# Performance work log

Hardware: AMD Instinct MI355X
Metric: run time of the kernel (lower is better)

The kernel has to match this reference:

```python
import jax, jax.numpy as jnp
import numpy as np


def _gather_nbrs(atoms, edges):
    # atoms [B,N,F], edges [B,N,D] (neighbor indices) -> [B,N,D,F]
    return jax.vmap(lambda a, e: a[e])(atoms, edges)


def _linear(x, W, b):
    return x @ W + b


def setup_inputs() -> dict:
    key = jax.random.key(0)
    ks = jax.random.split(key, 32)
    B, Nm, Dm, Fa, Fb = 64, 64, 6, 37, 6      # molecules
    Np, Dp, Fp = 512, 12, 480                  # proteins
    HM, HP, NC = 128, 128, 1

    def rn(k, shape):
        return jax.random.normal(k, shape, jnp.float32) * 0.05

    return {
        'm_atoms': jax.random.normal(ks[0], (B, Nm, Fa), jnp.float32),
        'm_bonds': jax.random.normal(ks[1], (B, Nm, Dm, Fb), jnp.float32),
        'm_edges': jax.random.randint(ks[2], (B, Nm, Dm), 0, Nm, jnp.int32),
        'p_atoms': jax.random.normal(ks[3], (B, Np, Fp), jnp.float32),
        'p_edges': jax.random.randint(ks[4], (B, Np, Dp), 0, Np, jnp.int32),
        # GraphConv mol 1: in 43 = 37 atom + 6 bond
        'W1': rn(ks[5], (43, 128)), 'b1': jnp.zeros((128,), jnp.float32),
        # GraphConv mol 2: in 134 = 128 + 6
        'W2': rn(ks[6], (134, 128)), 'b2': jnp.zeros((128,), jnp.float32),
        # GraphConv_p 1/2
        'Wp1': rn(ks[7], (480, 200)), 'bp1': jnp.zeros((200,), jnp.float32),
        'Wp2': rn(ks[8], (200, 100)), 'bp2': jnp.zeros((100,), jnp.float32),
        # GraphOutput (134 -> hid_dim_m), GraphOutput_p (100 -> hid_dim_p)
        'Wo': rn(ks[9], (134, HM)), 'bo': jnp.zeros((HM,), jnp.float32),
        'Wop': rn(ks[10], (100, HP)), 'bop': jnp.zeros((HP,), jnp.float32),
        # FC stack
        'Wf1': rn(ks[11], (HM + HP, 100)), 'bf1': jnp.zeros((100,), jnp.float32),
        'Wf2': rn(ks[12], (100, 100)), 'bf2': jnp.zeros((100,), jnp.float32),
        'Wout': rn(ks[13], (100, NC)), 'bout': jnp.zeros((NC,), jnp.float32),
    }


def reference(m_atoms, m_bonds, m_edges, p_atoms, p_edges,
              W1, b1, W2, b2, Wp1, bp1, Wp2, bp2,
              Wo, bo, Wop, bop, Wf1, bf1, Wf2, bf2, Wout, bout):
    def gconv_mol(atoms, W, b):
        # self + summed-neighbor atom features, concat summed bond features
        nbr_sum = _gather_nbrs(atoms, m_edges).sum(2)           # [B,N,F]
        summed = jnp.concatenate([atoms + nbr_sum, m_bonds.sum(2)], axis=-1)
        return _linear(summed, W, b)

    def gconv_pro(atoms, W, b):
        nbr_sum = _gather_nbrs(atoms, p_edges).sum(2)
        return _linear(atoms + nbr_sum, W, b)

    a = jax.nn.relu(gconv_mol(m_atoms, W1, b1))
    a = jax.nn.relu(gconv_mol(a, W2, b2))
    # GraphOutput: tanh(linear(cat[atoms, bond_sum])) summed over atoms
    fp_m = jnp.tanh(_linear(jnp.concatenate([a, m_bonds.sum(2)], -1), Wo, bo)).sum(1)

    p = jax.nn.relu(gconv_pro(p_atoms, Wp1, bp1))
    p = jax.nn.relu(gconv_pro(p, Wp2, bp2))
    fp_p = jnp.tanh(_linear(p, Wop, bop)).sum(1)

    fp = jnp.concatenate([fp_m, fp_p], axis=1)
    # NOTE: source applies FC1 then FC2 with no activation in between
    fp = _linear(_linear(fp, Wf1, bf1), Wf2, bf2)
    return jax.nn.sigmoid(_linear(fp, Wout, bout))
```

## Files before the change

kernel.cpp:

```cpp
#include <hip/hip_runtime.h>
#include <cmath>

#define B   64
#define NM  64
#define DM  6
#define FA  37
#define FB  6
#define NP  512
#define DP  12
#define FPD 480
#define HM  128
#define HP  128

typedef _Float16 half8 __attribute__((ext_vector_type(8)));
typedef float f32x4 __attribute__((ext_vector_type(4)));

static const size_t OFF_FPP = 0;
static const size_t OFF_Z1  = OFF_FPP + (size_t)B*128;
static const size_t OFF_Z2  = OFF_Z1  + (size_t)32768*224/2;
static const size_t OFF_W16 = OFF_Z2  + (size_t)32768*128/2;
#define W16_WT1   0
#define W16_WT2   107520
#define W16_WTOP  136192
#define W16_MW1T  152576
#define W16_MW2T  160768
#define W16_MWOT  181248
#define W16_BP1   201728
#define W16_BP2   201952
#define W16_TOT   202080

__device__ __forceinline__ half8 load_a_frag(const float* p) {
    float4 f0 = *(const float4*)(p);
    float4 f1 = *(const float4*)(p + 4);
    half8 h;
    h[0] = (_Float16)f0.x; h[1] = (_Float16)f0.y; h[2] = (_Float16)f0.z; h[3] = (_Float16)f0.w;
    h[4] = (_Float16)f1.x; h[5] = (_Float16)f1.y; h[6] = (_Float16)f1.z; h[7] = (_Float16)f1.w;
    return h;
}

__global__ void k_prep(const float* __restrict__ Wp1, const float* __restrict__ Wp2,
                       const float* __restrict__ Wop,
                       const float* __restrict__ W1,  const float* __restrict__ W2,
                       const float* __restrict__ Wo,
                       const float* __restrict__ bp1, const float* __restrict__ bp2,
                       _Float16* __restrict__ w16) {
    int idx = blockIdx.x * 256 + threadIdx.x;
    if (idx < W16_WT2) {
        int n = idx / 480, k = idx % 480;
        w16[idx] = (n < 200) ? (_Float16)Wp1[k * 200 + n] : (_Float16)0.f;
    } else if (idx < W16_WTOP) {
        int r = idx - W16_WT2;
        int n = r / 224, k = r % 224;
        w16[idx] = (n < 100 && k < 200) ? (_Float16)Wp2[k * 100 + n] : (_Float16)0.f;
    } else if (idx < W16_MW1T) {
        int r = idx - W16_WTOP;
        int n = r >> 7, k = r & 127;
        w16[idx] = (k < 100) ? (_Float16)Wop[k * 128 + n] : (_Float16)0.f;
    } else if (idx < W16_MW2T) {
        int r = idx - W16_MW1T;
        int n = r >> 6, k = r & 63;
        w16[idx] = (k < 43) ? (_Float16)W1[k * 128 + n] : (_Float16)0.f;
    } else if (idx < W16_MWOT) {
        int r = idx - W16_MW2T;
        int n = r / 160, k = r % 160;
        w16[idx] = (k < 134) ? (_Float16)W2[k * 128 + n] : (_Float16)0.f;
    } else if (idx < W16_BP1) {
        int r = idx - W16_MWOT;
        int n = r / 160, k = r % 160;
        w16[idx] = (k < 134) ? (_Float16)Wo[k * 128 + n] : (_Float16)0.f;
    } else if (idx < W16_BP2) {
        int k = idx - W16_BP1;
        w16[idx] = (k < 200) ? (_Float16)bp1[k] : (_Float16)0.f;
    } else if (idx < W16_TOT) {
        int k = idx - W16_BP2;
        w16[idx] = (k < 100) ? (_Float16)bp2[k] : (_Float16)0.f;
    }
}

__global__ __launch_bounds__(256) void k_zp1(
        const float* __restrict__ A, const _Float16* __restrict__ Wt,
        _Float16* __restrict__ Z) {
    int tid = threadIdx.x, lane = tid & 63, wid = tid >> 6;
    int rw = wid & 1, cw = wid >> 1;
    int rbase = blockIdx.x * 32 + rw * 16;
    int cbase = cw * 112;
    int lr = lane & 15, q = lane >> 4, lkb = q * 8;
    f32x4 acc[7] = {};
    const float* Ar = A + (size_t)(rbase + lr) * FPD + lkb;
    for (int k0 = 0; k0 < FPD; k0 += 32) {
        half8 a = load_a_frag(Ar + k0);
        #pragma unroll
        for (int nt = 0; nt < 7; ++nt) {
            half8 b = *(const half8*)&Wt[(size_t)(cbase + nt * 16 + lr) * FPD + k0 + lkb];
            acc[nt] = __builtin_amdgcn_mfma_f32_16x16x32_f16(a, b, acc[nt], 0, 0, 0);
        }
    }
    int rj = q * 4;
    #pragma unroll
    for (int nt = 0; nt < 7; ++nt) {
        int col = cbase + nt * 16 + lr;
        #pragma unroll
        for (int j = 0; j < 4; ++j)
            Z[(size_t)(rbase + rj + j) * 224 + col] = (_Float16)acc[nt][j];
    }
}

__global__ __launch_bounds__(256) void k_zp2f(
        const _Float16* __restrict__ Z1, const int* __restrict__ edges,
        const _Float16* __restrict__ bp1h, const _Float16* __restrict__ Wt,
        _Float16* __restrict__ Z2) {
    int bid = blockIdx.x;
    int t = (bid & 7) * 64 + (bid >> 3);
    int tid = threadIdx.x, lane = tid & 63, wid = tid >> 6;
    int lr = lane & 15, q = lane >> 4, lkb = q * 8;
    int rbase = t * 64 + wid * 16;
    int gr = rbase + lr;
    int mb = gr >> 9, lrow = gr & 511;
    const int* ep = edges + (size_t)gr * DP;
    const _Float16* zb = Z1 + ((size_t)mb << 9) * 224;
    const _Float16* src[13];
    src[0] = zb + (size_t)lrow * 224;
    #pragma unroll
    for (int d = 0; d < 12; ++d) src[d + 1] = zb + (size_t)ep[d] * 224;

    f32x4 acc[7] = {};
    for (int k0 = 0; k0 < 224; k0 += 32) {
        int ko = k0 + lkb;
        half8 s = *(const half8*)(src[0] + ko);
        #pragma unroll
        for (int d = 1; d < 13; ++d) s = s + *(const half8*)(src[d] + ko);
        s = s + *(const half8*)(bp1h + ko);
        #pragma unroll
        for (int j = 0; j < 8; ++j) if (s[j] < (_Float16)0.f) s[j] = (_Float16)0.f;
        #pragma unroll
        for (int nt = 0; nt < 7; ++nt) {
            half8 b = *(const half8*)&Wt[(size_t)(nt * 16 + lr) * 224 + ko];
            acc[nt] = __builtin_amdgcn_mfma_f32_16x16x32_f16(s, b, acc[nt], 0, 0, 0);
        }
    }
    int rj = q * 4;
    #pragma unroll
    for (int nt = 0; nt < 7; ++nt) {
        int col = nt * 16 + lr;
        #pragma unroll
        for (int j = 0; j < 4; ++j)
            Z2[(size_t)(rbase + rj + j) * 128 + col] = (_Float16)acc[nt][j];
    }
}

__global__ __launch_bounds__(256) void k_pof(
        const _Float16* __restrict__ Z2, const int* __restrict__ edges,
        const _Float16* __restrict__ bp2h, const _Float16* __restrict__ Wt,
        const float* __restrict__ bop, float* __restrict__ fpp) {
    int bid = blockIdx.x;
    int t = (bid & 7) * 64 + (bid >> 3);
    int tid = threadIdx.x, lane = tid & 63, wid = tid >> 6;
    int lr = lane & 15, q = lane >> 4, lkb = q * 8;
    int rbase = t * 64 + wid * 16;
    int gr = rbase + lr;
    int mb = gr >> 9, lrow = gr & 511;
    const int* ep = edges + (size_t)gr * DP;
    const _Float16* zb = Z2 + ((size_t)mb << 9) * 128;
    const _Float16* src[13];
    src[0] = zb + (size_t)lrow * 128;
    #pragma unroll
    for (int d = 0; d < 12; ++d) src[d + 1] = zb + (size_t)ep[d] * 128;

    f32x4 acc[8] = {};
    for (int k0 = 0; k0 < 128; k0 += 32) {
        int ko = k0 + lkb;
        half8 s = *(const half8*)(src[0] + ko);
        #pragma unroll
        for (int d = 1; d < 13; ++d) s = s + *(const half8*)(src[d] + ko);
        s = s + *(const half8*)(bp2h + ko);
        #pragma unroll
        for (int j = 0; j < 8; ++j) if (s[j] < (_Float16)0.f) s[j] = (_Float16)0.f;
        #pragma unroll
        for (int nt = 0; nt < 8; ++nt) {
            half8 b = *(const half8*)&Wt[(size_t)(nt * 16 + lr) * 128 + ko];
            acc[nt] = __builtin_amdgcn_mfma_f32_16x16x32_f16(s, b, acc[nt], 0, 0, 0);
        }
    }
    #pragma unroll
    for (int nt = 0; nt < 8; ++nt) {
        int col = nt * 16 + lr;
        float bb = bop[col];
        float s = 0.f;
        #pragma unroll
        for (int j = 0; j < 4; ++j) s += tanhf(acc[nt][j] + bb);
        s += __shfl_xor(s, 16);
        s += __shfl_xor(s, 32);
        if (lane < 16) atomicAdd(&fpp[mb * 128 + col], s);
    }
}

#define P_ATOM 40
#define P_S1   72
#define P_A    136
#define P_S23  168
__global__ __launch_bounds__(512) void k_mol(
        const float* __restrict__ m_atoms, const float* __restrict__ m_bonds,
        const int* __restrict__ m_edges,
        const _Float16* __restrict__ W1t, const _Float16* __restrict__ W2t,
        const _Float16* __restrict__ Wot,
        const float* __restrict__ b1, const float* __restrict__ b2,
        const float* __restrict__ bo,
        const float* __restrict__ fpp,
        const float* __restrict__ Wf1, const float* __restrict__ bf1,
        const float* __restrict__ Wf2, const float* __restrict__ bf2,
        const float* __restrict__ Wout, const float* __restrict__ bout,
        float* __restrict__ out) {
    int b = blockIdx.x, tid = threadIdx.x;
    __shared__ __align__(16) float smem[11464];
    float*     atoms_sh = smem;
    _Float16*  a1  = (_Float16*)smem;
    _Float16*  S1  = (_Float16*)(smem + 4352);
    _Float16*  S23 = (_Float16*)(smem + 4352);
    float*     bond  = smem + 9728;
    int*       edg   = (int*)(smem + 10112);
    float*     red   = smem + 10496;
    float*     fcb   = smem + 11008;

    const float* ga = m_atoms + (size_t)b * NM * FA;
    for (int i = tid; i < NM * FA; i += 512)
        atoms_sh[(i / FA) * P_ATOM + (i % FA)] = ga[i];
    if (tid < NM * DM) edg[tid] = m_edges[b * NM * DM + tid];
    if (tid < NM * FB) {
        int r = tid / FB, j = tid % FB;
        float s = 0.f;
        #pragma unroll
        for (int d = 0; d < DM; ++d) s += m_bonds[((size_t)(b * NM + r) * DM + d) * FB + j];
        bond[tid] = s;
    }
    __syncthreads();

    for (int i = tid; i < 64 * 64; i += 512) {
        int r = i >> 6, k = i & 63;
        float v = 0.f;
        if (k < FA) {
            v = atoms_sh[r * P_ATOM + k];
            #pragma unroll
            for (int d = 0; d < DM; ++d) v += atoms_sh[edg[r * DM + d] * P_ATOM + k];
        } else if (k < FA + FB) {
            v = bond[r * FB + (k - FA)];
        }
        S1[r * P_S1 + k] = (_Float16)v;
    }
    __syncthreads();

    int lane = tid & 63, wid = tid >> 6;
    int rw = wid & 3, cw = wid >> 2;
    int rbase = rw * 16, cbase = cw * 64;
    int lr = lane & 15, lkb = (lane >> 4) * 8, rj = (lane >> 4) * 4;

    {
        f32x4 acc[4] = {};
        for (int k0 = 0; k0 < 64; k0 += 32) {
            half8 a = *(const half8*)&S1[(rbase + lr) * P_S1 + k0 + lkb];
            #pragma unroll
            for (int nt = 0; nt < 4; ++nt) {
                half8 bf = *(const half8*)&W1t[(cbase + nt * 16 + lr) * 64 + k0 + lkb];
                acc[nt] = __builtin_amdgcn_mfma_f32_16x16x32_f16(a, bf, acc[nt], 0, 0, 0);
            }
        }
        #pragma unroll
        for (int nt = 0; nt < 4; ++nt) {
            int col = cbase + nt * 16 + lr;
            float bb = b1[col];
            #pragma unroll
            for (int j = 0; j < 4; ++j)
                a1[(rbase + rj + j) * P_A + col] = (_Float16)fmaxf(acc[nt][j] + bb, 0.f);
        }
    }
    __syncthreads();

    for (int i = tid; i < 64 * 160; i += 512) {
        int r = i / 160, k = i % 160;
        float v = 0.f;
        if (k < 128) {
            v = (float)a1[r * P_A + k];
            #pragma unroll
            for (int d = 0; d < DM; ++d) v += (float)a1[edg[r * DM + d] * P_A + k];
        } else if (k < 134) {
            v = bond[r * FB + (k - 128)];
        }
        S23[r * P_S23 + k] = (_Float16)v;
    }
    __syncthreads();

    f32x4 acc2[4] = {};
    for (int k0 = 0; k0 < 160; k0 += 32) {
        half8 a = *(const half8*)&S23[(rbase + lr) * P_S23 + k0 + lkb];
        #pragma unroll
        for (int nt = 0; nt < 4; ++nt) {
            half8 bf = *(const half8*)&W2t[(cbase + nt * 16 + lr) * 160 + k0 + lkb];
            acc2[nt] = __builtin_amdgcn_mfma_f32_16x16x32_f16(a, bf, acc2[nt], 0, 0, 0);
        }
    }
    __syncthreads();

    #pragma unroll
    for (int nt = 0; nt < 4; ++nt) {
        int col = cbase + nt * 16 + lr;
        float bb = b2[col];
        #pragma unroll
        for (int j = 0; j < 4; ++j)
            S23[(rbase + rj + j) * P_S23 + col] = (_Float16)fmaxf(acc2[nt][j] + bb, 0.f);
    }
    for (int i = tid; i < 64 * 32; i += 512) {
        int r = i >> 5, k = 128 + (i & 31);
        S23[r * P_S23 + k] = (k < 134) ? (_Float16)bond[r * FB + (k - 128)] : (_Float16)0.f;
    }
    __syncthreads();

    {
        f32x4 acc3[4] = {};
        for (int k0 = 0; k0 < 160; k0 += 32) {
            half8 a = *(const half8*)&S23[(rbase + lr) * P_S23 + k0 + lkb];
            #pragma unroll
            for (int nt = 0; nt < 4; ++nt) {
                half8 bf = *(const half8*)&Wot[(cbase + nt * 16 + lr) * 160 + k0 + lkb];
                acc3[nt] = __builtin_amdgcn_mfma_f32_16x16x32_f16(a, bf, acc3[nt], 0, 0, 0);
            }
        }
        #pragma unroll
        for (int nt = 0; nt < 4; ++nt) {
            int col = cbase + nt * 16 + lr;
            float bb = bo[col];
            float s = 0.f;
            #pragma unroll
            for (int j = 0; j < 4; ++j) s += tanhf(acc3[nt][j] + bb);
            s += __shfl_xor(s, 16);
            s += __shfl_xor(s, 32);
            if (lane < 16) red[rw * 128 + col] = s;
        }
    }
    __syncthreads();

    if (tid < 128)       fcb[tid] = red[tid] + red[128 + tid] + red[256 + tid] + red[384 + tid];
    else if (tid < 256)  fcb[tid] = fpp[b * 128 + (tid - 128)];
    __syncthreads();
    if (tid < 100) {
        float acc = bf1[tid];
        for (int k = 0; k < 256; ++k) acc = fmaf(fcb[k], Wf1[k * 100 + tid], acc);
        fcb[256 + tid] = acc;
    }
    __syncthreads();
    if (tid < 100) {
        float acc = bf2[tid];
        for (int k = 0; k < 100; ++k) acc = fmaf(fcb[256 + k], Wf2[k * 100 + tid], acc);
        fcb[356 + tid] = acc;
    }
    __syncthreads();
    if (tid < 64) {
        float v = fcb[356 + tid] * Wout[tid];
        if (tid + 64 < 100) v += fcb[356 + tid + 64] * Wout[tid + 64];
        #pragma unroll
        for (int off = 32; off > 0; off >>= 1) v += __shfl_down(v, off);
        if (tid == 0) out[b] = 1.f / (1.f + expf(-(v + bout[0])));
    }
}

extern "C" void kernel_launch(void* const* d_in, const int* in_sizes, int n_in,
                              void* d_out, int out_size, void* d_ws, size_t ws_size,
                              hipStream_t stream) {
    const float* m_atoms = (const float*)d_in[0];
    const float* m_bonds = (const float*)d_in[1];
    const int*   m_edges = (const int*)  d_in[2];
    const float* p_atoms = (const float*)d_in[3];
    const int*   p_edges = (const int*)  d_in[4];
    const float* W1   = (const float*)d_in[5];  const float* b1   = (const float*)d_in[6];
    const float* W2   = (const float*)d_in[7];  const float* b2   = (const float*)d_in[8];
    const float* Wp1  = (const float*)d_in[9];  const float* bp1  = (const float*)d_in[10];
    const float* Wp2  = (const float*)d_in[11]; const float* bp2  = (const float*)d_in[12];
    const float* Wo   = (const float*)d_in[13]; const float* bo   = (const float*)d_in[14];
    const float* Wop  = (const float*)d_in[15]; const float* bop  = (const float*)d_in[16];
    const float* Wf1  = (const float*)d_in[17]; const float* bf1  = (const float*)d_in[18];
    const float* Wf2  = (const float*)d_in[19]; const float* bf2  = (const float*)d_in[20];
    const float* Wout = (const float*)d_in[21]; const float* bout = (const float*)d_in[22];

    float* ws   = (float*)d_ws;
    float* fpp  = ws + OFF_FPP;
    _Float16* z1  = (_Float16*)(ws + OFF_Z1);
    _Float16* z2  = (_Float16*)(ws + OFF_Z2);
    _Float16* w16 = (_Float16*)(ws + OFF_W16);

    hipMemsetAsync(fpp, 0, (size_t)B * 128 * sizeof(float), stream);
    k_prep<<<dim3((W16_TOT + 255) / 256), 256, 0, stream>>>(
        Wp1, Wp2, Wop, W1, W2, Wo, bp1, bp2, w16);

    k_zp1 <<<dim3(B * NP / 32), 256, 0, stream>>>(p_atoms, w16 + W16_WT1, z1);
    k_zp2f<<<dim3(B * NP / 64), 256, 0, stream>>>(z1, p_edges, w16 + W16_BP1,
                                                  w16 + W16_WT2, z2);
    k_pof <<<dim3(B * NP / 64), 256, 0, stream>>>(z2, p_edges, w16 + W16_BP2,
                                                  w16 + W16_WTOP, bop, fpp);

    k_mol <<<dim3(B), 512, 0, stream>>>(m_atoms, m_bonds, m_edges,
                                        w16 + W16_MW1T, w16 + W16_MW2T, w16 + W16_MWOT,
                                        b1, b2, bo, fpp,
                                        Wf1, bf1, Wf2, bf2, Wout, bout, (float*)d_out);
}
```

Before: 260.7 us.

## Tile-swizzle protein weights, pad Z1 stride, split gather GEMMs across waves

```diff
diff --git a/kernel.cpp b/kernel.cpp
--- a/kernel.cpp
+++ b/kernel.cpp
@@ -17,7 +17,7 @@
 
 static const size_t OFF_FPP = 0;
 static const size_t OFF_Z1  = OFF_FPP + (size_t)B*128;
-static const size_t OFF_Z2  = OFF_Z1  + (size_t)32768*224/2;
+static const size_t OFF_Z2  = OFF_Z1  + (size_t)32768*256/2;
 static const size_t OFF_W16 = OFF_Z2  + (size_t)32768*128/2;
 #define W16_WT1   0
 #define W16_WT2   107520
@@ -29,9 +29,7 @@
 #define W16_BP2   201952
 #define W16_TOT   202080
 
-__device__ __forceinline__ half8 load_a_frag(const float* p) {
-    float4 f0 = *(const float4*)(p);
-    float4 f1 = *(const float4*)(p + 4);
+__device__ __forceinline__ half8 cvt8(float4 f0, float4 f1) {
     half8 h;
     h[0] = (_Float16)f0.x; h[1] = (_Float16)f0.y; h[2] = (_Float16)f0.z; h[3] = (_Float16)f0.w;
     h[4] = (_Float16)f1.x; h[5] = (_Float16)f1.y; h[6] = (_Float16)f1.z; h[7] = (_Float16)f1.w;
@@ -46,15 +44,21 @@
                        _Float16* __restrict__ w16) {
     int idx = blockIdx.x * 256 + threadIdx.x;
     if (idx < W16_WT2) {
-        int n = idx / 480, k = idx % 480;
+        int c = idx / 7168, r = idx % 7168;
+        int nt = r >> 9, lr = (r >> 5) & 15, kin = r & 31;
+        int n = nt * 16 + lr, k = c * 32 + kin;
         w16[idx] = (n < 200) ? (_Float16)Wp1[k * 200 + n] : (_Float16)0.f;
     } else if (idx < W16_WTOP) {
-        int r = idx - W16_WT2;
-        int n = r / 224, k = r % 224;
+        int r0 = idx - W16_WT2;
+        int c = r0 >> 12, r = r0 & 4095;
+        int nt = r >> 9, lr = (r >> 5) & 15, kin = r & 31;
+        int n = nt * 16 + lr, k = c * 32 + kin;
         w16[idx] = (n < 100 && k < 200) ? (_Float16)Wp2[k * 100 + n] : (_Float16)0.f;
     } else if (idx < W16_MW1T) {
-        int r = idx - W16_WTOP;
-        int n = r >> 7, k = r & 127;
+        int r0 = idx - W16_WTOP;
+        int c = r0 >> 12, r = r0 & 4095;
+        int nt = r >> 9, lr = (r >> 5) & 15, kin = r & 31;
+        int n = nt * 16 + lr, k = c * 32 + kin;
         w16[idx] = (k < 100) ? (_Float16)Wop[k * 128 + n] : (_Float16)0.f;
     } else if (idx < W16_MW2T) {
         int r = idx - W16_MW1T;
@@ -83,25 +87,32 @@
     int tid = threadIdx.x, lane = tid & 63, wid = tid >> 6;
     int rw = wid & 1, cw = wid >> 1;
     int rbase = blockIdx.x * 32 + rw * 16;
-    int cbase = cw * 112;
-    int lr = lane & 15, q = lane >> 4, lkb = q * 8;
+    int lr = lane & 15, q = lane >> 4;
     f32x4 acc[7] = {};
-    const float* Ar = A + (size_t)(rbase + lr) * FPD + lkb;
-    for (int k0 = 0; k0 < FPD; k0 += 32) {
-        half8 a = load_a_frag(Ar + k0);
+    const float* Ar = A + (size_t)(rbase + lr) * FPD + q * 8;
+    const _Float16* Wb = Wt + (size_t)(cw * 7) * 512 + lr * 32 + q * 8;
+    float4 a0 = *(const float4*)(Ar);
+    float4 a1 = *(const float4*)(Ar + 4);
+    for (int c = 0; c < 15; ++c) {
+        int cn = (c < 14) ? c + 1 : 14;
+        float4 na0 = *(const float4*)(Ar + cn * 32);
+        float4 na1 = *(const float4*)(Ar + cn * 32 + 4);
+        half8 a = cvt8(a0, a1);
+        const _Float16* wc = Wb + (size_t)c * 7168;
         #pragma unroll
         for (int nt = 0; nt < 7; ++nt) {
-            half8 b = *(const half8*)&Wt[(size_t)(cbase + nt * 16 + lr) * FPD + k0 + lkb];
+            half8 b = *(const half8*)(wc + nt * 512);
             acc[nt] = __builtin_amdgcn_mfma_f32_16x16x32_f16(a, b, acc[nt], 0, 0, 0);
         }
-    }
-    int rj = q * 4;
+        a0 = na0; a1 = na1;
+    }
+    int rj = q * 4, cbase = cw * 112;
     #pragma unroll
     for (int nt = 0; nt < 7; ++nt) {
         int col = cbase + nt * 16 + lr;
         #pragma unroll
         for (int j = 0; j < 4; ++j)
-            Z[(size_t)(rbase + rj + j) * 224 + col] = (_Float16)acc[nt][j];
+            Z[(size_t)(rbase + rj + j) * 256 + col] = (_Float16)acc[nt][j];
     }
 }
 
@@ -110,38 +121,52 @@
         const _Float16* __restrict__ bp1h, const _Float16* __restrict__ Wt,
         _Float16* __restrict__ Z2) {
     int bid = blockIdx.x;
-    int t = (bid & 7) * 64 + (bid >> 3);
+    int t = (bid & 7) * 128 + (bid >> 3);
     int tid = threadIdx.x, lane = tid & 63, wid = tid >> 6;
-    int lr = lane & 15, q = lane >> 4, lkb = q * 8;
-    int rbase = t * 64 + wid * 16;
+    int rw = wid & 1, cw = wid >> 1;
+    int lr = lane & 15, q = lane >> 4;
+    int rbase = t * 32 + rw * 16;
     int gr = rbase + lr;
     int mb = gr >> 9, lrow = gr & 511;
     const int* ep = edges + (size_t)gr * DP;
-    const _Float16* zb = Z1 + ((size_t)mb << 9) * 224;
+    const _Float16* zb = Z1 + (((size_t)mb << 9) << 8);
     const _Float16* src[13];
-    src[0] = zb + (size_t)lrow * 224;
-    #pragma unroll
-    for (int d = 0; d < 12; ++d) src[d + 1] = zb + (size_t)ep[d] * 224;
-
-    f32x4 acc[7] = {};
-    for (int k0 = 0; k0 < 224; k0 += 32) {
-        int ko = k0 + lkb;
-        half8 s = *(const half8*)(src[0] + ko);
-        #pragma unroll
-        for (int d = 1; d < 13; ++d) s = s + *(const half8*)(src[d] + ko);
-        s = s + *(const half8*)(bp1h + ko);
+    src[0] = zb + ((size_t)lrow << 8) + q * 8;
+    #pragma unroll
+    for (int d = 0; d < 12; ++d) src[d + 1] = zb + ((size_t)ep[d] << 8) + q * 8;
+
+    f32x4 acc[4] = {};
+    for (int c = 0; c < 7; ++c) {
+        int ko = c * 32;
+        half8 t0  = *(const half8*)(src[0]  + ko);
+        half8 t1  = *(const half8*)(src[1]  + ko);
+        half8 t2  = *(const half8*)(src[2]  + ko);
+        half8 t3  = *(const half8*)(src[3]  + ko);
+        half8 t4  = *(const half8*)(src[4]  + ko);
+        half8 t5  = *(const half8*)(src[5]  + ko);
+        half8 t6  = *(const half8*)(src[6]  + ko);
+        half8 t7  = *(const half8*)(src[7]  + ko);
+        half8 t8  = *(const half8*)(src[8]  + ko);
+        half8 t9  = *(const half8*)(src[9]  + ko);
+        half8 t10 = *(const half8*)(src[10] + ko);
+        half8 t11 = *(const half8*)(src[11] + ko);
+        half8 t12 = *(const half8*)(src[12] + ko);
+        half8 bb  = *(const half8*)(bp1h + ko + q * 8);
+        half8 s = (((t0 + t1) + (t2 + t3)) + ((t4 + t5) + (t6 + t7)))
+                + (((t8 + t9) + (t10 + t11)) + (t12 + bb));
         #pragma unroll
         for (int j = 0; j < 8; ++j) if (s[j] < (_Float16)0.f) s[j] = (_Float16)0.f;
-        #pragma unroll
-        for (int nt = 0; nt < 7; ++nt) {
-            half8 b = *(const half8*)&Wt[(size_t)(nt * 16 + lr) * 224 + ko];
+        const _Float16* wc = Wt + (size_t)(c * 8 + cw * 4) * 512 + lr * 32 + q * 8;
+        #pragma unroll
+        for (int nt = 0; nt < 4; ++nt) {
+            half8 b = *(const half8*)(wc + nt * 512);
             acc[nt] = __builtin_amdgcn_mfma_f32_16x16x32_f16(s, b, acc[nt], 0, 0, 0);
         }
     }
-    int rj = q * 4;
-    #pragma unroll
-    for (int nt = 0; nt < 7; ++nt) {
-        int col = nt * 16 + lr;
+    int rj = q * 4, cbase = cw * 64;
+    #pragma unroll
+    for (int nt = 0; nt < 4; ++nt) {
+        int col = cbase + nt * 16 + lr;
         #pragma unroll
         for (int j = 0; j < 4; ++j)
             Z2[(size_t)(rbase + rj + j) * 128 + col] = (_Float16)acc[nt][j];
@@ -153,37 +178,52 @@
         const _Float16* __restrict__ bp2h, const _Float16* __restrict__ Wt,
         const float* __restrict__ bop, float* __restrict__ fpp) {
     int bid = blockIdx.x;
-    int t = (bid & 7) * 64 + (bid >> 3);
+    int t = (bid & 7) * 128 + (bid >> 3);
     int tid = threadIdx.x, lane = tid & 63, wid = tid >> 6;
-    int lr = lane & 15, q = lane >> 4, lkb = q * 8;
-    int rbase = t * 64 + wid * 16;
+    int rw = wid & 1, cw = wid >> 1;
+    int lr = lane & 15, q = lane >> 4;
+    int rbase = t * 32 + rw * 16;
     int gr = rbase + lr;
     int mb = gr >> 9, lrow = gr & 511;
     const int* ep = edges + (size_t)gr * DP;
-    const _Float16* zb = Z2 + ((size_t)mb << 9) * 128;
+    const _Float16* zb = Z2 + (((size_t)mb << 9) << 7);
     const _Float16* src[13];
-    src[0] = zb + (size_t)lrow * 128;
-    #pragma unroll
-    for (int d = 0; d < 12; ++d) src[d + 1] = zb + (size_t)ep[d] * 128;
-
-    f32x4 acc[8] = {};
-    for (int k0 = 0; k0 < 128; k0 += 32) {
-        int ko = k0 + lkb;
-        half8 s = *(const half8*)(src[0] + ko);
-        #pragma unroll
-        for (int d = 1; d < 13; ++d) s = s + *(const half8*)(src[d] + ko);
-        s = s + *(const half8*)(bp2h + ko);
+    src[0] = zb + ((size_t)lrow << 7) + q * 8;
+    #pragma unroll
+    for (int d = 0; d < 12; ++d) src[d + 1] = zb + ((size_t)ep[d] << 7) + q * 8;
+
+    f32x4 acc[4] = {};
+    for (int c = 0; c < 4; ++c) {
+        int ko = c * 32;
+        half8 t0  = *(const half8*)(src[0]  + ko);
+        half8 t1  = *(const half8*)(src[1]  + ko);
+        half8 t2  = *(const half8*)(src[2]  + ko);
+        half8 t3  = *(const half8*)(src[3]  + ko);
+        half8 t4  = *(const half8*)(src[4]  + ko);
+        half8 t5  = *(const half8*)(src[5]  + ko);
+        half8 t6  = *(const half8*)(src[6]  + ko);
+        half8 t7  = *(const half8*)(src[7]  + ko);
+        half8 t8  = *(const half8*)(src[8]  + ko);
+        half8 t9  = *(const half8*)(src[9]  + ko);
+        half8 t10 = *(const half8*)(src[10] + ko);
+        half8 t11 = *(const half8*)(src[11] + ko);
+        half8 t12 = *(const half8*)(src[12] + ko);
+        half8 bb  = *(const half8*)(bp2h + ko + q * 8);
+        half8 s = (((t0 + t1) + (t2 + t3)) + ((t4 + t5) + (t6 + t7)))
+                + (((t8 + t9) + (t10 + t11)) + (t12 + bb));
         #pragma unroll
         for (int j = 0; j < 8; ++j) if (s[j] < (_Float16)0.f) s[j] = (_Float16)0.f;
-        #pragma unroll
-        for (int nt = 0; nt < 8; ++nt) {
-            half8 b = *(const half8*)&Wt[(size_t)(nt * 16 + lr) * 128 + ko];
+        const _Float16* wc = Wt + (size_t)(c * 8 + cw * 4) * 512 + lr * 32 + q * 8;
+        #pragma unroll
+        for (int nt = 0; nt < 4; ++nt) {
+            half8 b = *(const half8*)(wc + nt * 512);
             acc[nt] = __builtin_amdgcn_mfma_f32_16x16x32_f16(s, b, acc[nt], 0, 0, 0);
         }
     }
-    #pragma unroll
-    for (int nt = 0; nt < 8; ++nt) {
-        int col = nt * 16 + lr;
+    int cbase = cw * 64;
+    #pragma unroll
+    for (int nt = 0; nt < 4; ++nt) {
+        int col = cbase + nt * 16 + lr;
         float bb = bop[col];
         float s = 0.f;
         #pragma unroll
@@ -390,9 +430,9 @@
         Wp1, Wp2, Wop, W1, W2, Wo, bp1, bp2, w16);
 
     k_zp1 <<<dim3(B * NP / 32), 256, 0, stream>>>(p_atoms, w16 + W16_WT1, z1);
-    k_zp2f<<<dim3(B * NP / 64), 256, 0, stream>>>(z1, p_edges, w16 + W16_BP1,
+    k_zp2f<<<dim3(B * NP / 32), 256, 0, stream>>>(z1, p_edges, w16 + W16_BP1,
                                                   w16 + W16_WT2, z2);
-    k_pof <<<dim3(B * NP / 64), 256, 0, stream>>>(z2, p_edges, w16 + W16_BP2,
+    k_pof <<<dim3(B * NP / 32), 256, 0, stream>>>(z2, p_edges, w16 + W16_BP2,
                                                   w16 + W16_WTOP, bop, fpp);
 
     k_mol <<<dim3(B), 512, 0, stream>>>(m_atoms, m_bonds, m_edges,
```

Measured after the change: 288.4 us. 1.11x slower.
